# Performance work log

Hardware: AMD Instinct MI355X
Metric: run time of the kernel (lower is better)

Reference implementation:

```python
import jax, jax.numpy as jnp
import numpy as np

B, S, HIDDEN = 2, 2048, 2048
NUM_HEADS = 16
HEAD_DIM = 128
ROPE_BASE = 10000.0


def _rope_cos_sin(positions):
    # positions: [B, S] int -> cos/sin [B, 1, S, HEAD_DIM]
    inv_freq = 1.0 / (ROPE_BASE ** (jnp.arange(0, HEAD_DIM, 2, dtype=jnp.float32) / HEAD_DIM))
    freqs = positions.astype(jnp.float32)[..., None] * inv_freq  # [B, S, D/2]
    emb = jnp.concatenate([freqs, freqs], axis=-1)  # [B, S, D]
    return jnp.cos(emb)[:, None, :, :], jnp.sin(emb)[:, None, :, :]


def _rotate_half(x, cos, sin):
    half = x.shape[-1] // 2
    x1, x2 = x[..., :half], x[..., half:]
    return jnp.concatenate([-x2, x1], axis=-1) * sin + x * cos


def setup_inputs() -> dict:
    key = jax.random.key(0)
    ks = jax.random.split(key, 6)
    hidden_states = jax.random.normal(ks[0], (B, S, HIDDEN), dtype=jnp.float32)
    positions = jnp.arange(B * S, dtype=jnp.int64 if jax.config.x64_enabled else jnp.int32).reshape(B, S)
    scale = 0.02
    Wq = jax.random.normal(ks[1], (HIDDEN, NUM_HEADS * HEAD_DIM), dtype=jnp.float32) * scale
    Wk = jax.random.normal(ks[2], (HIDDEN, NUM_HEADS * HEAD_DIM), dtype=jnp.float32) * scale
    Wv = jax.random.normal(ks[3], (HIDDEN, NUM_HEADS * HEAD_DIM), dtype=jnp.float32) * scale
    Wo = jax.random.normal(ks[4], (NUM_HEADS * HEAD_DIM, HIDDEN), dtype=jnp.float32) * scale
    bq = jnp.zeros((NUM_HEADS * HEAD_DIM,), dtype=jnp.float32)
    bk = jnp.zeros((NUM_HEADS * HEAD_DIM,), dtype=jnp.float32)
    bv = jnp.zeros((NUM_HEADS * HEAD_DIM,), dtype=jnp.float32)
    return {"positions": positions, "hidden_states": hidden_states,
            "Wq": Wq, "bq": bq, "Wk": Wk, "bk": bk, "Wv": Wv, "bv": bv, "Wo": Wo}


def reference(positions, hidden_states, Wq, bq, Wk, bk, Wv, bv, Wo):
    b, s, _ = hidden_states.shape
    # projections
    q = hidden_states @ Wq + bq  # [B, S, H*D]
    k = hidden_states @ Wk + bk
    v = hidden_states @ Wv + bv
    # -> [B, H, S, D]
    q = q.reshape(b, s, NUM_HEADS, HEAD_DIM).transpose(0, 2, 1, 3)
    k = k.reshape(b, s, NUM_HEADS, HEAD_DIM).transpose(0, 2, 1, 3)
    v = v.reshape(b, s, NUM_HEADS, HEAD_DIM).transpose(0, 2, 1, 3)
    # RoPE
    cos, sin = _rope_cos_sin(positions)
    q = _rotate_half(q, cos, sin)
    k = _rotate_half(k, cos, sin)
    # scaled dot-product attention (no mask)
    scaling = HEAD_DIM ** -0.5
    scores = jnp.einsum('bhqd,bhkd->bhqk', q, k) * scaling
    attn = jax.nn.softmax(scores, axis=-1)
    out = jnp.einsum('bhqk,bhkd->bhqd', attn, v)
    out = out.transpose(0, 2, 1, 3).reshape(b, s, NUM_HEADS * HEAD_DIM)
    return out @ Wo
```

## Files before the change

### kernel.cpp

```cpp
#include <hip/hip_runtime.h>
#include <cstdint>
#include <cstddef>

typedef unsigned short u16;
typedef __attribute__((ext_vector_type(8))) unsigned short u16x8;
typedef __attribute__((ext_vector_type(8))) short bf16x8;
typedef __attribute__((ext_vector_type(4))) float f32x4;

#define MFMA_BF16(a, b, c) __builtin_amdgcn_mfma_f32_16x16x32_bf16((a), (b), (c), 0, 0, 0)

__device__ __forceinline__ u16 f2bf(float f) {
  union { float f; uint32_t u; } v; v.f = f;
  uint32_t r = v.u + 0x7fffu + ((v.u >> 16) & 1u);
  return (u16)(r >> 16);
}
__device__ __forceinline__ float bf2f(u16 u) {
  union { uint32_t u; float f; } v; v.u = ((uint32_t)u) << 16;
  return v.f;
}
__device__ __forceinline__ void gl2lds16(const void* g, void* l) {
  __builtin_amdgcn_global_load_lds((__attribute__((address_space(1))) const void*)g,
                                   (__attribute__((address_space(3))) void*)l, 16, 0, 0);
}


__global__ __launch_bounds__(256) void cvt_kernel(const float* __restrict__ in,
                                                  u16* __restrict__ out) {
  int idx = blockIdx.x * 256 + threadIdx.x;
  float4 a = ((const float4*)in)[(size_t)idx * 2];
  float4 b = ((const float4*)in)[(size_t)idx * 2 + 1];
  u16x8 o;
  o[0] = f2bf(a.x); o[1] = f2bf(a.y); o[2] = f2bf(a.z); o[3] = f2bf(a.w);
  o[4] = f2bf(b.x); o[5] = f2bf(b.y); o[6] = f2bf(b.z); o[7] = f2bf(b.w);
  *(u16x8*)(out + (size_t)idx * 8) = o;
}

__global__ __launch_bounds__(256) void trans_kernel(const float* __restrict__ in,
                                                    u16* __restrict__ out) {
  __shared__ float tile[64][65];
  int t = threadIdx.x;
  int r0 = blockIdx.y * 64, c0 = blockIdx.x * 64;
#pragma unroll
  for (int i = 0; i < 16; ++i) {
    int idx = i * 256 + t; int r = idx >> 6, c = idx & 63;
    tile[r][c] = in[(size_t)(r0 + r) * 2048 + c0 + c];
  }
  __syncthreads();
#pragma unroll
  for (int i = 0; i < 16; ++i) {
    int idx = i * 256 + t; int r = idx >> 6, c = idx & 63;
    out[(size_t)(c0 + r) * 2048 + r0 + c] = f2bf(tile[c][r]);
  }
}

__global__ __launch_bounds__(256) void rope_table_kernel(const int* __restrict__ pos,
                                                         float* __restrict__ cosT,
                                                         float* __restrict__ sinT) {
  int idx = blockIdx.x * 256 + threadIdx.x;
  int i = idx & 63, t = idx >> 6;
  double ang = (double)pos[t] * exp(-(double)i * (9.210340371976184 / 64.0));
  cosT[idx] = (float)cos(ang);
  sinT[idx] = (float)sin(ang);
}

__global__ __launch_bounds__(256) void rope_kernel(u16* __restrict__ Q,
                                                   u16* __restrict__ Kk,
                                                   const float* __restrict__ cosT,
                                                   const float* __restrict__ sinT) {
  int idx = blockIdx.x * 256 + threadIdx.x;
  int d = idx & 63, h = (idx >> 6) & 15, tok = idx >> 10;
  int b = tok >> 11, s = tok & 2047;
  size_t base = ((size_t)((b * 16 + h) * 2048 + s)) * 128;
  float c = cosT[(tok << 6) + d], sn = sinT[(tok << 6) + d];
  const float sc = 0.08838834764831845f;
  float q1 = bf2f(Q[base + d]), q2 = bf2f(Q[base + d + 64]);
  Q[base + d]      = f2bf((q1 * c - q2 * sn) * sc);
  Q[base + d + 64] = f2bf((q2 * c + q1 * sn) * sc);
  float k1 = bf2f(Kk[base + d]), k2 = bf2f(Kk[base + d + 64]);
  Kk[base + d]      = f2bf(k1 * c - k2 * sn);
  Kk[base + d + 64] = f2bf(k2 * c + k1 * sn);
}

__global__ __launch_bounds__(256) void vtrans_kernel(const u16* __restrict__ V,
                                                     u16* __restrict__ Vt) {
  __shared__ u16 tile[128][72];
  int t = threadIdx.x;
  int bh = blockIdx.x >> 5, st = blockIdx.x & 31;
  const u16* src = V + ((size_t)bh * 2048 + st * 64) * 128;
#pragma unroll
  for (int i = 0; i < 4; ++i) {
    int idx = i * 256 + t;
    int s = idx >> 4;
    int d0 = (idx & 15) << 3;
    u16x8 v = *(const u16x8*)(src + (size_t)s * 128 + d0);
#pragma unroll
    for (int j = 0; j < 8; ++j) tile[d0 + j][s] = v[j];
  }
  __syncthreads();
  u16* dst = Vt + (size_t)bh * 128 * 2048 + st * 64;
#pragma unroll
  for (int i = 0; i < 4; ++i) {
    int idx = i * 256 + t;
    int d = idx >> 3;
    int s0 = (idx & 7) << 3;
    u16x8 o;
#pragma unroll
    for (int j = 0; j < 8; ++j) o[j] = tile[d][s0 + j];
    *(u16x8*)(dst + (size_t)d * 2048 + s0) = o;
  }
}


__global__ __launch_bounds__(256) void gemm1_kernel(
    const u16* __restrict__ A,
    const u16* __restrict__ Bt,
    const float* __restrict__ bq, const float* __restrict__ bk, const float* __restrict__ bv,
    u16* __restrict__ Qo, u16* __restrict__ Ko, u16* __restrict__ Vo) {
  __shared__ u16 sA[128 * 32], sB[128 * 32];
  const int K = 2048;
  int t = threadIdx.x, lane = t & 63, wid = t >> 6;
  int bm = blockIdx.x & 31, bn = blockIdx.x >> 5;
  int m0 = bm << 7, n0 = bn << 7;
  int wr = wid >> 1, wc = wid & 1;
  int fr = lane & 15, fq = lane >> 4;

  const f32x4 vzero = {0.f, 0.f, 0.f, 0.f};
  f32x4 acc[4][4];
#pragma unroll
  for (int m = 0; m < 4; ++m)
#pragma unroll
    for (int n = 0; n < 4; ++n) acc[m][n] = vzero;

  int arow = t >> 2, acol = (t & 3) << 3;
  const u16* ga0 = A + (size_t)(m0 + arow) * K + acol;
  const u16* ga1 = ga0 + (size_t)64 * K;
  const u16* gb0 = Bt + (size_t)(n0 + arow) * K + acol;
  const u16* gb1 = gb0 + (size_t)64 * K;
  u16* lA0 = sA + t * 8; u16* lA1 = sA + 2048 + t * 8;
  u16* lB0 = sB + t * 8; u16* lB1 = sB + 2048 + t * 8;

  for (int k0 = 0; k0 < K; k0 += 32) {
    gl2lds16(ga0 + k0, lA0);
    gl2lds16(ga1 + k0, lA1);
    gl2lds16(gb0 + k0, lB0);
    gl2lds16(gb1 + k0, lB1);
    __syncthreads();
    bf16x8 af[4], bfv[4];
#pragma unroll
    for (int m = 0; m < 4; ++m)
      af[m] = *(const bf16x8*)(sA + ((wr * 64 + m * 16 + fr) * 32 + fq * 8));
#pragma unroll
    for (int n = 0; n < 4; ++n)
      bfv[n] = *(const bf16x8*)(sB + ((wc * 64 + n * 16 + fr) * 32 + fq * 8));
#pragma unroll
    for (int m = 0; m < 4; ++m)
#pragma unroll
      for (int n = 0; n < 4; ++n)
        acc[m][n] = MFMA_BF16(af[m], bfv[n], acc[m][n]);
    __syncthreads();
  }
#pragma unroll
  for (int n = 0; n < 4; ++n) {
    int col = n0 + wc * 64 + n * 16 + fr;
    int which = col >> 11;
    int cin = col & 2047;
    const float* bp = (which == 0) ? bq : (which == 1) ? bk : bv;
    u16* dst = (which == 0) ? Qo : (which == 1) ? Ko : Vo;
    float bias = bp[cin];
    int h = cin >> 7, d = cin & 127;
#pragma unroll
    for (int m = 0; m < 4; ++m) {
      int row = m0 + wr * 64 + m * 16 + fq * 4;
#pragma unroll
      for (int r = 0; r < 4; ++r) {
        int tok = row + r;
        int b = tok >> 11, s = tok & 2047;
        dst[((size_t)((b * 16 + h) * 2048 + s) << 7) + d] = f2bf(acc[m][n][r] + bias);
      }
    }
  }
}

__global__ __launch_bounds__(256) void gemm2_kernel(
    const u16* __restrict__ A,
    const u16* __restrict__ Bt,
    float* __restrict__ C) {
  __shared__ u16 sA[128 * 32], sB[128 * 32];
  const int K = 2048;
  int t = threadIdx.x, lane = t & 63, wid = t >> 6;
  int bm = blockIdx.x & 31, bn = blockIdx.x >> 5;
  int m0 = bm << 7, n0 = bn << 7;
  int wr = wid >> 1, wc = wid & 1;
  int fr = lane & 15, fq = lane >> 4;

  const f32x4 vzero = {0.f, 0.f, 0.f, 0.f};
  f32x4 acc[4][4];
#pragma unroll
  for (int m = 0; m < 4; ++m)
#pragma unroll
    for (int n = 0; n < 4; ++n) acc[m][n] = vzero;

  int arow = t >> 2, acol = (t & 3) << 3;
  const u16* ga0 = A + (size_t)(m0 + arow) * K + acol;
  const u16* ga1 = ga0 + (size_t)64 * K;
  const u16* gb0 = Bt + (size_t)(n0 + arow) * K + acol;
  const u16* gb1 = gb0 + (size_t)64 * K;
  u16* lA0 = sA + t * 8; u16* lA1 = sA + 2048 + t * 8;
  u16* lB0 = sB + t * 8; u16* lB1 = sB + 2048 + t * 8;

  for (int k0 = 0; k0 < K; k0 += 32) {
    gl2lds16(ga0 + k0, lA0);
    gl2lds16(ga1 + k0, lA1);
    gl2lds16(gb0 + k0, lB0);
    gl2lds16(gb1 + k0, lB1);
    __syncthreads();
    bf16x8 af[4], bfv[4];
#pragma unroll
    for (int m = 0; m < 4; ++m)
      af[m] = *(const bf16x8*)(sA + ((wr * 64 + m * 16 + fr) * 32 + fq * 8));
#pragma unroll
    for (int n = 0; n < 4; ++n)
      bfv[n] = *(const bf16x8*)(sB + ((wc * 64 + n * 16 + fr) * 32 + fq * 8));
#pragma unroll
    for (int m = 0; m < 4; ++m)
#pragma unroll
      for (int n = 0; n < 4; ++n)
        acc[m][n] = MFMA_BF16(af[m], bfv[n], acc[m][n]);
    __syncthreads();
  }
#pragma unroll
  for (int n = 0; n < 4; ++n) {
    int col = n0 + wc * 64 + n * 16 + fr;
#pragma unroll
    for (int m = 0; m < 4; ++m) {
      int row = m0 + wr * 64 + m * 16 + fq * 4;
#pragma unroll
      for (int r = 0; r < 4; ++r)
        C[(size_t)(row + r) * 2048 + col] = acc[m][n][r];
    }
  }
}

__global__ __launch_bounds__(256) void attn_kernel(
    const u16* __restrict__ Q_,
    const u16* __restrict__ K_,
    const u16* __restrict__ Vt_,
    u16* __restrict__ AO) {
  __shared__ u16 sK[64 * 128];
  __shared__ u16 sV[128 * 64];
  __shared__ u16 sP[4 * 16 * 64];
  int t = threadIdx.x, lane = t & 63, wid = t >> 6;
  int fr = lane & 15, fq = lane >> 4;
  int qt = blockIdx.x & 31, bh = blockIdx.x >> 5;
  int q0 = qt << 6;
  const u16* Qb = Q_ + (size_t)bh * 2048 * 128;
  const char* Kc = (const char*)(K_ + (size_t)bh * 2048 * 128);
  const char* Vc = (const char*)(Vt_ + (size_t)bh * 128 * 2048);

  bf16x8 qf[4];
  {
    const u16* qp = Qb + (size_t)(q0 + wid * 16 + fr) * 128 + fq * 8;
#pragma unroll
    for (int kk = 0; kk < 4; ++kk) qf[kk] = *(const bf16x8*)(qp + kk * 32);
  }

  const char* kg[4]; char* kl[4];
  const char* vg[4]; char* vl[4];
#pragma unroll
  for (int i = 0; i < 4; ++i) {
    int kr = i * 16 + (t >> 4);
    kg[i] = Kc + (size_t)kr * 256 + (((t & 15) << 4) ^ ((kr & 7) << 4));
    kl[i] = (char*)sK + i * 4096 + t * 16;
    int vr = i * 32 + (t >> 3);
    vg[i] = Vc + (size_t)vr * 4096 + (((t & 7) << 4) ^ ((vr & 7) << 4));
    vl[i] = (char*)sV + i * 4096 + t * 16;
  }

  float mrun[4], lrun[4];
#pragma unroll
  for (int r = 0; r < 4; ++r) { mrun[r] = -1e30f; lrun[r] = 0.f; }
  const f32x4 vzero = {0.f, 0.f, 0.f, 0.f};
  f32x4 oacc[8];
#pragma unroll
  for (int fd = 0; fd < 8; ++fd) oacc[fd] = vzero;

  char* sPw = (char*)(sP + wid * 1024);

  for (int kv0 = 0; kv0 < 2048; kv0 += 64) {
#pragma unroll
    for (int i = 0; i < 4; ++i) gl2lds16(kg[i] + (size_t)kv0 * 256, kl[i]);
#pragma unroll
    for (int i = 0; i < 4; ++i) gl2lds16(vg[i] + (size_t)kv0 * 2, vl[i]);
    __syncthreads();

    f32x4 sacc[4];
#pragma unroll
    for (int n = 0; n < 4; ++n) sacc[n] = vzero;
#pragma unroll
    for (int n = 0; n < 4; ++n) {
      int krow = n * 16 + fr;
      int swz = (krow & 7) << 4;
      const char* kbase = (const char*)sK + krow * 256;
#pragma unroll
      for (int kk = 0; kk < 4; ++kk) {
        bf16x8 kf = *(const bf16x8*)(kbase + ((kk * 64 + fq * 16) ^ swz));
        sacc[n] = MFMA_BF16(qf[kk], kf, sacc[n]);
      }
    }

    float scl[4];
#pragma unroll
    for (int r = 0; r < 4; ++r) {
      float v = fmaxf(fmaxf(sacc[0][r], sacc[1][r]), fmaxf(sacc[2][r], sacc[3][r]));
      v = fmaxf(v, __shfl_xor(v, 1));
      v = fmaxf(v, __shfl_xor(v, 2));
      v = fmaxf(v, __shfl_xor(v, 4));
      v = fmaxf(v, __shfl_xor(v, 8));
      float mn = fmaxf(mrun[r], v);
      scl[r] = __expf(mrun[r] - mn);
      mrun[r] = mn;
    }
    float rs[4] = {0.f, 0.f, 0.f, 0.f};
#pragma unroll
    for (int n = 0; n < 4; ++n) {
#pragma unroll
      for (int r = 0; r < 4; ++r) {
        float p = __expf(sacc[n][r] - mrun[r]);
        rs[r] += p;
        int prow = fq * 4 + r;
        *(u16*)(sPw + prow * 128 + ((((n * 16 + fr) << 1)) ^ ((prow & 7) << 4))) = f2bf(p);
      }
    }
#pragma unroll
    for (int r = 0; r < 4; ++r) {
      float s = rs[r];
      s += __shfl_xor(s, 1);
      s += __shfl_xor(s, 2);
      s += __shfl_xor(s, 4);
      s += __shfl_xor(s, 8);
      lrun[r] = lrun[r] * scl[r] + s;
    }
#pragma unroll
    for (int fd = 0; fd < 8; ++fd)
#pragma unroll
      for (int r = 0; r < 4; ++r) oacc[fd][r] *= scl[r];

    bf16x8 pf[2];
#pragma unroll
    for (int kk = 0; kk < 2; ++kk)
      pf[kk] = *(const bf16x8*)(sPw + fr * 128 + ((kk * 64 + fq * 16) ^ ((fr & 7) << 4)));
#pragma unroll
    for (int fd = 0; fd < 8; ++fd) {
      int vrow = fd * 16 + fr;
      int swz = (vrow & 7) << 4;
      const char* vbase = (const char*)sV + vrow * 128;
#pragma unroll
      for (int kk = 0; kk < 2; ++kk) {
        bf16x8 vf = *(const bf16x8*)(vbase + ((kk * 64 + fq * 16) ^ swz));
        oacc[fd] = MFMA_BF16(pf[kk], vf, oacc[fd]);
      }
    }
    __syncthreads();
  }

  int h = bh & 15, b = bh >> 4;
#pragma unroll
  for (int fd = 0; fd < 8; ++fd) {
    int col = h * 128 + fd * 16 + fr;
#pragma unroll
    for (int r = 0; r < 4; ++r) {
      int tok = b * 2048 + q0 + wid * 16 + fq * 4 + r;
      AO[(size_t)tok * 2048 + col] = f2bf(oacc[fd][r] / lrun[r]);
    }
  }
}


extern "C" void kernel_launch(void* const* d_in, const int* in_sizes, int n_in,
                              void* d_out, int out_size, void* d_ws, size_t ws_size,
                              hipStream_t stream) {
  (void)in_sizes; (void)n_in; (void)out_size; (void)ws_size;
  const int*   positions = (const int*)d_in[0];
  const float* hidden    = (const float*)d_in[1];
  const float* Wq = (const float*)d_in[2];
  const float* bq = (const float*)d_in[3];
  const float* Wk = (const float*)d_in[4];
  const float* bk = (const float*)d_in[5];
  const float* Wv = (const float*)d_in[6];
  const float* bv = (const float*)d_in[7];
  const float* Wo = (const float*)d_in[8];
  float* out = (float*)d_out;

  char* ws = (char*)d_ws;
  u16*   Xb   = (u16*)(ws);
  u16*   Wt   = (u16*)(ws + 16777216);
  u16*   Wot  = (u16*)(ws + 41943040);
  u16*   Qb   = (u16*)(ws + 50331648);
  u16*   Kb   = (u16*)(ws + 67108864);
  u16*   Vb   = (u16*)(ws + 83886080);
  u16*   Vtb  = (u16*)(ws + 100663296);
  u16*   AO   = (u16*)(ws + 117440512);
  float* cosT = (float*)(ws + 134217728);
  float* sinT = (float*)(ws + 135266304);

  cvt_kernel<<<4096, 256, 0, stream>>>(hidden, Xb);
  trans_kernel<<<dim3(32, 32), 256, 0, stream>>>(Wq, Wt);
  trans_kernel<<<dim3(32, 32), 256, 0, stream>>>(Wk, Wt + (size_t)2048 * 2048);
  trans_kernel<<<dim3(32, 32), 256, 0, stream>>>(Wv, Wt + (size_t)2 * 2048 * 2048);
  trans_kernel<<<dim3(32, 32), 256, 0, stream>>>(Wo, Wot);
  rope_table_kernel<<<1024, 256, 0, stream>>>(positions, cosT, sinT);
  gemm1_kernel<<<1536, 256, 0, stream>>>(Xb, Wt, bq, bk, bv, Qb, Kb, Vb);
  rope_kernel<<<16384, 256, 0, stream>>>(Qb, Kb, cosT, sinT);
  vtrans_kernel<<<1024, 256, 0, stream>>>(Vb, Vtb);
  attn_kernel<<<1024, 256, 0, stream>>>(Qb, Kb, Vtb, AO);
  gemm2_kernel<<<512, 256, 0, stream>>>(AO, Wot, out);
}
```

Baseline: 509.9 us.

## Double-buffer attention KV tiles, widen query tile, lazy rescale, XCD-aware block remap

```diff
diff --git a/kernel.cpp b/kernel.cpp
--- a/kernel.cpp
+++ b/kernel.cpp
@@ -59,8 +59,10 @@
   int idx = blockIdx.x * 256 + threadIdx.x;
   int i = idx & 63, t = idx >> 6;
   double ang = (double)pos[t] * exp(-(double)i * (9.210340371976184 / 64.0));
-  cosT[idx] = (float)cos(ang);
-  sinT[idx] = (float)sin(ang);
+  double s, c;
+  sincos(ang, &s, &c);
+  cosT[idx] = (float)c;
+  sinT[idx] = (float)s;
 }
 
 __global__ __launch_bounds__(256) void rope_kernel(u16* __restrict__ Q,
@@ -119,7 +121,8 @@
   __shared__ u16 sA[128 * 32], sB[128 * 32];
   const int K = 2048;
   int t = threadIdx.x, lane = t & 63, wid = t >> 6;
-  int bm = blockIdx.x & 31, bn = blockIdx.x >> 5;
+  int bid = (blockIdx.x & 7) * 192 + (blockIdx.x >> 3);
+  int bm = bid & 31, bn = bid >> 5;
   int m0 = bm << 7, n0 = bn << 7;
   int wr = wid >> 1, wc = wid & 1;
   int fr = lane & 15, fq = lane >> 4;
@@ -188,7 +191,8 @@
   __shared__ u16 sA[128 * 32], sB[128 * 32];
   const int K = 2048;
   int t = threadIdx.x, lane = t & 63, wid = t >> 6;
-  int bm = blockIdx.x & 31, bn = blockIdx.x >> 5;
+  int bid = (blockIdx.x & 7) * 64 + (blockIdx.x >> 3);
+  int bm = bid & 31, bn = bid >> 5;
   int m0 = bm << 7, n0 = bn << 7;
   int wr = wid >> 1, wc = wid & 1;
   int fr = lane & 15, fq = lane >> 4;
@@ -246,133 +250,186 @@
     const u16* __restrict__ K_,
     const u16* __restrict__ Vt_,
     u16* __restrict__ AO) {
-  __shared__ u16 sK[64 * 128];
-  __shared__ u16 sV[128 * 64];
-  __shared__ u16 sP[4 * 16 * 64];
+  __shared__ u16 sK[2][64 * 128];
+  __shared__ u16 sV[2][128 * 64];
+  __shared__ u16 sP[4][32 * 64];
   int t = threadIdx.x, lane = t & 63, wid = t >> 6;
   int fr = lane & 15, fq = lane >> 4;
-  int qt = blockIdx.x & 31, bh = blockIdx.x >> 5;
-  int q0 = qt << 6;
+  int bid = (blockIdx.x & 7) * 64 + (blockIdx.x >> 3);
+  int qt = bid & 15, bh = bid >> 4;
+  int q0 = qt << 7;
   const u16* Qb = Q_ + (size_t)bh * 2048 * 128;
   const char* Kc = (const char*)(K_ + (size_t)bh * 2048 * 128);
   const char* Vc = (const char*)(Vt_ + (size_t)bh * 128 * 2048);
 
-  bf16x8 qf[4];
-  {
-    const u16* qp = Qb + (size_t)(q0 + wid * 16 + fr) * 128 + fq * 8;
-#pragma unroll
-    for (int kk = 0; kk < 4; ++kk) qf[kk] = *(const bf16x8*)(qp + kk * 32);
-  }
-
-  const char* kg[4]; char* kl[4];
-  const char* vg[4]; char* vl[4];
+  bf16x8 qf[2][4];
+#pragma unroll
+  for (int m = 0; m < 2; ++m) {
+    const u16* qp = Qb + (size_t)(q0 + wid * 32 + m * 16 + fr) * 128 + fq * 8;
+#pragma unroll
+    for (int kk = 0; kk < 4; ++kk) qf[m][kk] = *(const bf16x8*)(qp + kk * 32);
+  }
+
+  int kgoff[4], kldst[4], vgoff[4], vldst[4];
 #pragma unroll
   for (int i = 0; i < 4; ++i) {
     int kr = i * 16 + (t >> 4);
-    kg[i] = Kc + (size_t)kr * 256 + (((t & 15) << 4) ^ ((kr & 7) << 4));
-    kl[i] = (char*)sK + i * 4096 + t * 16;
+    kgoff[i] = kr * 256 + (((t & 15) << 4) ^ ((kr & 7) << 4));
+    kldst[i] = i * 4096 + t * 16;
     int vr = i * 32 + (t >> 3);
-    vg[i] = Vc + (size_t)vr * 4096 + (((t & 7) << 4) ^ ((vr & 7) << 4));
-    vl[i] = (char*)sV + i * 4096 + t * 16;
-  }
-
-  float mrun[4], lrun[4];
-#pragma unroll
-  for (int r = 0; r < 4; ++r) { mrun[r] = -1e30f; lrun[r] = 0.f; }
+    vgoff[i] = vr * 4096 + (((t & 7) << 4) ^ ((vr & 7) << 4));
+    vldst[i] = i * 4096 + t * 16;
+  }
+
+#define STAGE(tt, bb)                                                          \
+  {                                                                            \
+    size_t ko = (size_t)(tt) * 64 * 256;                                       \
+    size_t vo = (size_t)(tt) * 128;                                            \
+    _Pragma("unroll")                                                          \
+    for (int i = 0; i < 4; ++i)                                                \
+      gl2lds16(Kc + ko + kgoff[i], (char*)sK[bb] + kldst[i]);                  \
+    _Pragma("unroll")                                                          \
+    for (int i = 0; i < 4; ++i)                                                \
+      gl2lds16(Vc + vo + vgoff[i], (char*)sV[bb] + vldst[i]);                  \
+  }
+
+  float mrun[2][4], lrun[2][4];
+#pragma unroll
+  for (int m = 0; m < 2; ++m)
+#pragma unroll
+    for (int r = 0; r < 4; ++r) { mrun[m][r] = -1e30f; lrun[m][r] = 0.f; }
   const f32x4 vzero = {0.f, 0.f, 0.f, 0.f};
-  f32x4 oacc[8];
-#pragma unroll
-  for (int fd = 0; fd < 8; ++fd) oacc[fd] = vzero;
-
-  char* sPw = (char*)(sP + wid * 1024);
-
-  for (int kv0 = 0; kv0 < 2048; kv0 += 64) {
-#pragma unroll
-    for (int i = 0; i < 4; ++i) gl2lds16(kg[i] + (size_t)kv0 * 256, kl[i]);
-#pragma unroll
-    for (int i = 0; i < 4; ++i) gl2lds16(vg[i] + (size_t)kv0 * 2, vl[i]);
-    __syncthreads();
-
-    f32x4 sacc[4];
-#pragma unroll
-    for (int n = 0; n < 4; ++n) sacc[n] = vzero;
+  f32x4 oacc[2][8];
+#pragma unroll
+  for (int m = 0; m < 2; ++m)
+#pragma unroll
+    for (int fd = 0; fd < 8; ++fd) oacc[m][fd] = vzero;
+
+  char* sPw = (char*)sP[wid];
+
+  STAGE(0, 0);
+  __syncthreads();
+
+  for (int tile = 0; tile < 32; ++tile) {
+    int cur = tile & 1;
+    if (tile < 31) STAGE(tile + 1, cur ^ 1);
+    const char* Kb_ = (const char*)sK[cur];
+    const char* Vb_ = (const char*)sV[cur];
+
+    f32x4 sacc[2][4];
+#pragma unroll
+    for (int m = 0; m < 2; ++m)
+#pragma unroll
+      for (int n = 0; n < 4; ++n) sacc[m][n] = vzero;
+    __builtin_amdgcn_s_setprio(1);
 #pragma unroll
     for (int n = 0; n < 4; ++n) {
       int krow = n * 16 + fr;
       int swz = (krow & 7) << 4;
-      const char* kbase = (const char*)sK + krow * 256;
+      const char* kbase = Kb_ + krow * 256;
 #pragma unroll
       for (int kk = 0; kk < 4; ++kk) {
         bf16x8 kf = *(const bf16x8*)(kbase + ((kk * 64 + fq * 16) ^ swz));
-        sacc[n] = MFMA_BF16(qf[kk], kf, sacc[n]);
-      }
-    }
-
-    float scl[4];
-#pragma unroll
-    for (int r = 0; r < 4; ++r) {
-      float v = fmaxf(fmaxf(sacc[0][r], sacc[1][r]), fmaxf(sacc[2][r], sacc[3][r]));
-      v = fmaxf(v, __shfl_xor(v, 1));
-      v = fmaxf(v, __shfl_xor(v, 2));
-      v = fmaxf(v, __shfl_xor(v, 4));
-      v = fmaxf(v, __shfl_xor(v, 8));
-      float mn = fmaxf(mrun[r], v);
-      scl[r] = __expf(mrun[r] - mn);
-      mrun[r] = mn;
-    }
-    float rs[4] = {0.f, 0.f, 0.f, 0.f};
-#pragma unroll
-    for (int n = 0; n < 4; ++n) {
+        sacc[0][n] = MFMA_BF16(qf[0][kk], kf, sacc[0][n]);
+        sacc[1][n] = MFMA_BF16(qf[1][kk], kf, sacc[1][n]);
+      }
+    }
+    __builtin_amdgcn_s_setprio(0);
+
+    float pmax[2][4];
+#pragma unroll
+    for (int m = 0; m < 2; ++m)
 #pragma unroll
       for (int r = 0; r < 4; ++r) {
-        float p = __expf(sacc[n][r] - mrun[r]);
-        rs[r] += p;
-        int prow = fq * 4 + r;
-        *(u16*)(sPw + prow * 128 + ((((n * 16 + fr) << 1)) ^ ((prow & 7) << 4))) = f2bf(p);
-      }
-    }
-#pragma unroll
-    for (int r = 0; r < 4; ++r) {
-      float s = rs[r];
-      s += __shfl_xor(s, 1);
-      s += __shfl_xor(s, 2);
-      s += __shfl_xor(s, 4);
-      s += __shfl_xor(s, 8);
-      lrun[r] = lrun[r] * scl[r] + s;
-    }
-#pragma unroll
-    for (int fd = 0; fd < 8; ++fd)
-#pragma unroll
-      for (int r = 0; r < 4; ++r) oacc[fd][r] *= scl[r];
-
-    bf16x8 pf[2];
-#pragma unroll
-    for (int kk = 0; kk < 2; ++kk)
-      pf[kk] = *(const bf16x8*)(sPw + fr * 128 + ((kk * 64 + fq * 16) ^ ((fr & 7) << 4)));
+        float v = fmaxf(fmaxf(sacc[m][0][r], sacc[m][1][r]),
+                        fmaxf(sacc[m][2][r], sacc[m][3][r]));
+        v = fmaxf(v, __shfl_xor(v, 1));
+        v = fmaxf(v, __shfl_xor(v, 2));
+        v = fmaxf(v, __shfl_xor(v, 4));
+        v = fmaxf(v, __shfl_xor(v, 8));
+        pmax[m][r] = v;
+      }
+    int ok = 1;
+#pragma unroll
+    for (int m = 0; m < 2; ++m)
+#pragma unroll
+      for (int r = 0; r < 4; ++r)
+        ok &= (pmax[m][r] <= mrun[m][r] + 8.f) ? 1 : 0;
+    if (!__all(ok)) {
+#pragma unroll
+      for (int m = 0; m < 2; ++m)
+#pragma unroll
+        for (int r = 0; r < 4; ++r) {
+          float mn = fmaxf(mrun[m][r], pmax[m][r]);
+          float scl = __expf(mrun[m][r] - mn);
+          mrun[m][r] = mn;
+          lrun[m][r] *= scl;
+#pragma unroll
+          for (int fd = 0; fd < 8; ++fd) oacc[m][fd][r] *= scl;
+        }
+    }
+    float rs[2][4] = {{0.f, 0.f, 0.f, 0.f}, {0.f, 0.f, 0.f, 0.f}};
+#pragma unroll
+    for (int m = 0; m < 2; ++m)
+#pragma unroll
+      for (int n = 0; n < 4; ++n)
+#pragma unroll
+        for (int r = 0; r < 4; ++r) {
+          float p = __expf(sacc[m][n][r] - mrun[m][r]);
+          rs[m][r] += p;
+          int q = m * 16 + fq * 4 + r;
+          *(u16*)(sPw + q * 128 + ((((n * 16 + fr) << 1)) ^ ((q & 7) << 4))) = f2bf(p);
+        }
+#pragma unroll
+    for (int m = 0; m < 2; ++m)
+#pragma unroll
+      for (int r = 0; r < 4; ++r) {
+        float s = rs[m][r];
+        s += __shfl_xor(s, 1);
+        s += __shfl_xor(s, 2);
+        s += __shfl_xor(s, 4);
+        s += __shfl_xor(s, 8);
+        lrun[m][r] += s;
+      }
+
+    bf16x8 pf[2][2];
+#pragma unroll
+    for (int m = 0; m < 2; ++m)
+#pragma unroll
+      for (int kk = 0; kk < 2; ++kk)
+        pf[m][kk] = *(const bf16x8*)(sPw + (m * 16 + fr) * 128 +
+                                     ((kk * 64 + fq * 16) ^ ((fr & 7) << 4)));
+    __builtin_amdgcn_s_setprio(1);
 #pragma unroll
     for (int fd = 0; fd < 8; ++fd) {
       int vrow = fd * 16 + fr;
-      int swz = (vrow & 7) << 4;
-      const char* vbase = (const char*)sV + vrow * 128;
+      int vswz = (vrow & 7) << 4;
+      const char* vbase = Vb_ + vrow * 128;
 #pragma unroll
       for (int kk = 0; kk < 2; ++kk) {
-        bf16x8 vf = *(const bf16x8*)(vbase + ((kk * 64 + fq * 16) ^ swz));
-        oacc[fd] = MFMA_BF16(pf[kk], vf, oacc[fd]);
-      }
-    }
+        bf16x8 vf = *(const bf16x8*)(vbase + ((kk * 64 + fq * 16) ^ vswz));
+        oacc[0][fd] = MFMA_BF16(pf[0][kk], vf, oacc[0][fd]);
+        oacc[1][fd] = MFMA_BF16(pf[1][kk], vf, oacc[1][fd]);
+      }
+    }
+    __builtin_amdgcn_s_setprio(0);
     __syncthreads();
   }
+#undef STAGE
 
   int h = bh & 15, b = bh >> 4;
 #pragma unroll
-  for (int fd = 0; fd < 8; ++fd) {
-    int col = h * 128 + fd * 16 + fr;
+  for (int m = 0; m < 2; ++m)
 #pragma unroll
     for (int r = 0; r < 4; ++r) {
-      int tok = b * 2048 + q0 + wid * 16 + fq * 4 + r;
-      AO[(size_t)tok * 2048 + col] = f2bf(oacc[fd][r] / lrun[r]);
-    }
-  }
+      float inv = 1.f / lrun[m][r];
+      int tok = b * 2048 + q0 + wid * 32 + m * 16 + fq * 4 + r;
+#pragma unroll
+      for (int fd = 0; fd < 8; ++fd) {
+        int col = h * 128 + fd * 16 + fr;
+        AO[(size_t)tok * 2048 + col] = f2bf(oacc[m][fd][r] * inv);
+      }
+    }
 }
 
 
@@ -412,6 +469,6 @@
   gemm1_kernel<<<1536, 256, 0, stream>>>(Xb, Wt, bq, bk, bv, Qb, Kb, Vb);
   rope_kernel<<<16384, 256, 0, stream>>>(Qb, Kb, cosT, sinT);
   vtrans_kernel<<<1024, 256, 0, stream>>>(Vb, Vtb);
-  attn_kernel<<<1024, 256, 0, stream>>>(Qb, Kb, Vtb, AO);
+  attn_kernel<<<512, 256, 0, stream>>>(Qb, Kb, Vtb, AO);
   gemm2_kernel<<<512, 256, 0, stream>>>(AO, Wot, out);
 }
```

After: 548.4 us. 7.6% more time.
